# Kernel optimization log

Hardware: AMD Instinct MI355X
Metric: run time of the kernel (lower is better)

Reference implementation:

```python
import jax, jax.numpy as jnp
import numpy as np
import math

DIM = 1024
N_HEAD = 16
HEAD_DIM = DIM // N_HEAD  # 64
B, T = 4, 2048


def rotate_half(x):
    # lucidrains-style interleaved rotation: (x1, x2) pairs -> (-x2, x1)
    x = x.reshape(*x.shape[:-1], -1, 2)
    x1, x2 = x[..., 0], x[..., 1]
    return jnp.stack((-x2, x1), axis=-1).reshape(*x.shape[:-2], -1)


def apply_rope(x):
    # x: [b, h, t, d]
    d = x.shape[-1]
    t = x.shape[-2]
    inv_freq = 1.0 / (10000.0 ** (jnp.arange(0, d, 2, dtype=jnp.float32) / d))  # [d/2]
    angles = jnp.arange(t, dtype=jnp.float32)[:, None] * inv_freq[None, :]      # [t, d/2]
    angles = jnp.repeat(angles, 2, axis=-1)                                     # [t, d] interleaved
    cos, sin = jnp.cos(angles), jnp.sin(angles)
    return x * cos + rotate_half(x) * sin


def setup_inputs() -> dict:
    key = jax.random.key(0)
    kx, kw1, kb1, kw2, kb2 = jax.random.split(key, 5)
    x = jax.random.normal(kx, (B, T, DIM), dtype=jnp.float32)
    mask = jnp.tril(jnp.ones((T, T), dtype=jnp.int32))  # causal
    s = 0.02
    qkv_w = jax.random.normal(kw1, (DIM, 3 * DIM), dtype=jnp.float32) * s
    qkv_b = jax.random.normal(kb1, (3 * DIM,), dtype=jnp.float32) * s
    out_w = jax.random.normal(kw2, (DIM, DIM), dtype=jnp.float32) * s
    out_b = jax.random.normal(kb2, (DIM,), dtype=jnp.float32) * s
    return {"x": x, "mask": mask, "qkv_w": qkv_w, "qkv_b": qkv_b,
            "out_w": out_w, "out_b": out_b}


def reference(x, mask, qkv_w, qkv_b, out_w, out_b):
    b, t, _ = x.shape
    qkv = x @ qkv_w + qkv_b                       # [b, t, 3*dim]
    q, k, v = jnp.split(qkv, 3, axis=-1)
    def to_heads(z):
        return z.reshape(b, t, N_HEAD, HEAD_DIM).transpose(0, 2, 1, 3)  # [b,h,t,d]
    q, k, v = to_heads(q), to_heads(k), to_heads(v)
    q = apply_rope(q)
    k = apply_rope(k)
    scores = jnp.einsum('bhqd,bhkd->bhqk', q, k) / math.sqrt(HEAD_DIM)
    scores = jnp.where(mask[None, None, :, :] == 0, -jnp.inf, scores)
    attn = jax.nn.softmax(scores, axis=-1)        # dropout = identity (eval)
    out = jnp.einsum('bhqk,bhkd->bhqd', attn, v)  # [b,h,t,d]
    out = out.transpose(0, 2, 1, 3).reshape(b, t, DIM)
    return out @ out_w + out_b
```

## Files before the change

kernel.cpp:

```cpp
#include <hip/hip_runtime.h>

typedef __bf16 bf16_t;
typedef __bf16 bf16x8 __attribute__((ext_vector_type(8)));
typedef float  f32x4  __attribute__((ext_vector_type(4)));
typedef float  f32x16 __attribute__((ext_vector_type(16)));
typedef unsigned u32x4 __attribute__((ext_vector_type(4)));

#define DIMM  1024
#define NHEAD 16
#define HDIM  64
#define BATCH 4
#define SEQ   2048
#define MROWS (BATCH*SEQ)

#define AQB   128
#define AKV   64
#define NP    (SEQ/AQB)
#define SKS   72
#define LOG2E 1.44269504088896f

__device__ __forceinline__ void gload_lds16(const bf16_t* g, bf16_t* l) {
  __builtin_amdgcn_global_load_lds(
      (const __attribute__((address_space(1))) void*)g,
      (__attribute__((address_space(3))) void*)l, 16, 0, 0);
}

__device__ __forceinline__ unsigned short f2bu(float f) {
  bf16_t b = (bf16_t)f;
  return __builtin_bit_cast(unsigned short, b);
}
__device__ __forceinline__ float bu2f(unsigned short u) {
  return __uint_as_float(((unsigned)u) << 16);
}
__device__ __forceinline__ unsigned packbf(float a, float b) {
  return (unsigned)f2bu(a) | ((unsigned)f2bu(b) << 16);
}
__device__ __forceinline__ float fexp2(float x) {
  float r; asm("v_exp_f32 %0, %1" : "=v"(r) : "v"(x)); return r;
}

__global__ void k_convert(const float* __restrict__ in, bf16_t* __restrict__ out, int n4) {
  int i = blockIdx.x * blockDim.x + threadIdx.x;
  if (i >= n4) return;
  float4 v = reinterpret_cast<const float4*>(in)[i];
  ushort4 o;
  o.x = f2bu(v.x); o.y = f2bu(v.y); o.z = f2bu(v.z); o.w = f2bu(v.w);
  reinterpret_cast<ushort4*>(out)[i] = o;
}

__global__ void k_transpose_convert(const float* __restrict__ in, bf16_t* __restrict__ out,
                                    int R, int C) {
  __shared__ float tile[32][33];
  int cb = blockIdx.x * 32, rb = blockIdx.y * 32;
  int tx = threadIdx.x, ty = threadIdx.y;
  #pragma unroll
  for (int i = 0; i < 4; ++i)
    tile[ty + i*8][tx] = in[(size_t)(rb + ty + i*8) * C + cb + tx];
  __syncthreads();
  #pragma unroll
  for (int i = 0; i < 4; ++i)
    out[(size_t)(cb + ty + i*8) * R + rb + tx] = (bf16_t)tile[tx][ty + i*8];
}

__global__ void k_rope_table(float* __restrict__ cosT, float* __restrict__ sinT) {
  int id = blockIdx.x * blockDim.x + threadIdx.x;
  if (id >= SEQ * 32) return;
  int t = id >> 5, i = id & 31;
  double ang = (double)t * pow(10000.0, -(double)i / 32.0);
  cosT[id] = (float)cos(ang);
  sinT[id] = (float)sin(ang);
}

__global__ __launch_bounds__(512, 2) void k_gemm0(
    const bf16_t* __restrict__ A, const bf16_t* __restrict__ BT,
    const float* __restrict__ bias,
    bf16_t* __restrict__ q, bf16_t* __restrict__ k, bf16_t* __restrict__ vt,
    const float* __restrict__ cosT, const float* __restrict__ sinT)
{
  __shared__ bf16_t sA[2][2][128 * 64];
  __shared__ bf16_t sB[2][2][128 * 64];

  const int tid = threadIdx.x;
  const int w = tid >> 6;
  const int lane = tid & 63;
  const int wm = w >> 2, wn = w & 3;
  const int l15 = lane & 15, l4 = lane >> 4;

  int nwg = gridDim.x * gridDim.y;
  int id  = blockIdx.y * gridDim.x + blockIdx.x;
  int cpx = nwg >> 3;
  int sid = (id & 7) * cpx + (id >> 3);
  int bx = sid % gridDim.x, by = sid / gridDim.x;
  const int rowA0 = by * 256, colB0 = bx * 256;

  f32x4 acc[8][4] = {};
  bf16x8 bf_[4];

  auto stage = [&](int tile, int part) {
    if (tile >= 16) return;
    const int kh = part >> 1;
    const bool isB = part & 1;
    const bf16_t* src = isB ? BT : A;
    const int r0 = isB ? colB0 : rowA0;
    bf16_t* dst = (isB ? &sB[0][0][0] : &sA[0][0][0]) + ((tile & 1) * 2 + kh) * (128 * 64);
    #pragma unroll
    for (int call = 0; call < 2; ++call) {
      int n = call * 512 + tid;
      int R = n >> 3, slot = n & 7;
      int sp = slot ^ (R & 7);
      int row = R * 2 + (sp >> 2);
      gload_lds16(src + (size_t)(r0 + row) * 1024 + tile * 64 + kh * 32 + (sp & 3) * 8,
                  dst + n * 8);
    }
  };

  auto rdA = [&](int bc, int kh, int mfa) -> bf16x8 {
    int row = wm * 128 + mfa * 16 + l15;
    int R = row >> 1;
    int slot = (((row & 1) << 2) | l4) ^ (R & 7);
    return *reinterpret_cast<const bf16x8*>(&sA[bc][kh][R * 64 + slot * 8]);
  };
  auto rdB = [&](int bc, int kh, int nf) -> bf16x8 {
    int row = wn * 64 + nf * 16 + l15;
    int R = row >> 1;
    int slot = (((row & 1) << 2) | l4) ^ (R & 7);
    return *reinterpret_cast<const bf16x8*>(&sB[bc][kh][R * 64 + slot * 8]);
  };

  auto phase = [&](int bc, int kh, int mh, int stile, int spart, int wait_n) {
    bf16x8 af[4];
    if (mh == 0) {
      #pragma unroll
      for (int nf = 0; nf < 4; ++nf) bf_[nf] = rdB(bc, kh, nf);
    }
    #pragma unroll
    for (int mf = 0; mf < 4; ++mf) af[mf] = rdA(bc, kh, mh * 4 + mf);
    stage(stile, spart);
    if (wait_n == 4)      asm volatile("s_waitcnt vmcnt(4)" ::: "memory");
    else if (wait_n == 0) asm volatile("s_waitcnt vmcnt(0)" ::: "memory");
    __builtin_amdgcn_s_barrier();
    __builtin_amdgcn_s_setprio(1);
    #pragma unroll
    for (int mf = 0; mf < 4; ++mf)
      #pragma unroll
      for (int nf = 0; nf < 4; ++nf)
        acc[mh * 4 + mf][nf] = __builtin_amdgcn_mfma_f32_16x16x32_bf16(
            af[mf], bf_[nf], acc[mh * 4 + mf][nf], 0, 0, 0);
    __builtin_amdgcn_s_setprio(0);
    __builtin_amdgcn_s_barrier();
  };

  stage(0, 0); stage(0, 1); stage(0, 2); stage(0, 3);
  stage(1, 0); stage(1, 1);
  asm volatile("s_waitcnt vmcnt(4)" ::: "memory");
  __builtin_amdgcn_s_barrier();

  for (int i = 0; i < 8; ++i) {
    const int t0 = 2 * i, t1 = 2 * i + 1;
    phase(0, 0, 0, t1,     2, -1);
    phase(0, 0, 1, t1,     3, -1);
    phase(0, 1, 0, t0 + 2, 0, -1);
    phase(0, 1, 1, t0 + 2, 1, (t0 + 2 < 16) ? 4 : 0);
    phase(1, 0, 0, t0 + 2, 2, -1);
    phase(1, 0, 1, t0 + 2, 3, -1);
    phase(1, 1, 0, t0 + 3, 0, -1);
    phase(1, 1, 1, t0 + 3, 1, (t0 + 3 < 16) ? 4 : 0);
  }

  const bool isV = (bx >= 8);
  const bool isQ = (bx < 4);
  const float qs = 0.125f * LOG2E;
  if (isV) {
    #pragma unroll
    for (int mfa = 0; mfa < 8; ++mfa) {
      #pragma unroll
      for (int nf = 0; nf < 4; ++nf) {
        int n = colB0 + wn * 64 + nf * 16 + l15;
        int h = (n >> 6) & 15, d = n & 63;
        float bs = bias[n];
        int m0 = rowA0 + wm * 128 + mfa * 16 + l4 * 4;
        int b = m0 >> 11, t = m0 & 2047;
        ushort4 pk;
        pk.x = f2bu(acc[mfa][nf][0] + bs);
        pk.y = f2bu(acc[mfa][nf][1] + bs);
        pk.z = f2bu(acc[mfa][nf][2] + bs);
        pk.w = f2bu(acc[mfa][nf][3] + bs);
        *reinterpret_cast<ushort4*>(
            vt + ((size_t)((b * NHEAD + h) * HDIM + d)) * SEQ + t) = pk;
      }
    }
  } else {
    bf16_t* dst = isQ ? q : k;
    #pragma unroll
    for (int mfa = 0; mfa < 8; ++mfa) {
      #pragma unroll
      for (int nf = 0; nf < 4; ++nf) {
        int n = colB0 + wn * 64 + nf * 16 + l15;
        int h = (n >> 6) & 15, d = n & 63;
        int i2 = d >> 1;
        float bs = bias[n];
        #pragma unroll
        for (int r = 0; r < 4; ++r) {
          int m = rowA0 + wm * 128 + mfa * 16 + l4 * 4 + r;
          int b = m >> 11, t = m & 2047;
          float val = acc[mfa][nf][r] + bs;
          float prt = __shfl_xor(val, 1);
          float c = cosT[(t << 5) + i2], s = sinT[(t << 5) + i2];
          float y = (d & 1) ? (val * c + prt * s) : (val * c - prt * s);
          if (isQ) y *= qs;
          dst[((size_t)(b * NHEAD + h) * SEQ + t) * HDIM + d] = (bf16_t)y;
        }
      }
    }
  }
}

__global__ __launch_bounds__(256) void k_gemm1(
    const bf16_t* __restrict__ A, const bf16_t* __restrict__ BT,
    const float* __restrict__ bias, float* __restrict__ outf, int M, int N, int K)
{
  __shared__ bf16_t sA[128 * 32];
  __shared__ bf16_t sB[128 * 32];
  const int tid = threadIdx.x;
  const int w = tid >> 6, lane = tid & 63;
  const int wr = w >> 1, wc = w & 1;
  const int l15 = lane & 15, l4 = lane >> 4;

  int nwg = gridDim.x * gridDim.y;
  int id  = blockIdx.y * gridDim.x + blockIdx.x;
  int cpx = nwg >> 3;
  int sid = (id & 7) * cpx + (id >> 3);
  int bx = sid % gridDim.x, by = sid / gridDim.x;

  const int rowA0 = by * 128;
  const int colB0 = bx * 128;

  f32x4 acc[4][4] = {};

  const int nkt = K >> 5;
  for (int kt = 0; kt < nkt; ++kt) {
    __syncthreads();
    #pragma unroll
    for (int i = 0; i < 2; ++i) {
      int c = i * 256 + w * 64 + lane;
      int row = c >> 2, k8 = (c & 3) * 8;
      gload_lds16(A  + (size_t)(rowA0 + row) * K + kt * 32 + k8, sA + (i * 256 + w * 64) * 8);
      gload_lds16(BT + (size_t)(colB0 + row) * K + kt * 32 + k8, sB + (i * 256 + w * 64) * 8);
    }
    asm volatile("s_waitcnt vmcnt(0)" ::: "memory");
    __syncthreads();
    bf16x8 af[4], bfr[4];
    #pragma unroll
    for (int mi = 0; mi < 4; ++mi)
      af[mi] = *reinterpret_cast<const bf16x8*>(sA + (wr * 64 + mi * 16 + l15) * 32 + l4 * 8);
    #pragma unroll
    for (int ni = 0; ni < 4; ++ni)
      bfr[ni] = *reinterpret_cast<const bf16x8*>(sB + (wc * 64 + ni * 16 + l15) * 32 + l4 * 8);
    #pragma unroll
    for (int mi = 0; mi < 4; ++mi)
      #pragma unroll
      for (int ni = 0; ni < 4; ++ni)
        acc[mi][ni] = __builtin_amdgcn_mfma_f32_16x16x32_bf16(af[mi], bfr[ni], acc[mi][ni], 0, 0, 0);
  }

  #pragma unroll
  for (int mi = 0; mi < 4; ++mi) {
    #pragma unroll
    for (int ni = 0; ni < 4; ++ni) {
      int n = colB0 + wc * 64 + ni * 16 + l15;
      float bs = bias[n];
      #pragma unroll
      for (int r = 0; r < 4; ++r) {
        int m = rowA0 + wr * 64 + mi * 16 + l4 * 4 + r;
        outf[(size_t)m * N + n] = acc[mi][ni][r] + bs;
      }
    }
  }
}

__global__ __launch_bounds__(256, 2) void k_attn(
    const bf16_t* __restrict__ Q, const bf16_t* __restrict__ Kb,
    const bf16_t* __restrict__ Vt, bf16_t* __restrict__ O)
{
  __shared__ bf16_t sK[2][64 * SKS];
  __shared__ bf16_t sV[2][64 * SKS];

  const int tid = threadIdx.x;
  const int w = tid >> 6, lane = tid & 63;
  const int l31 = lane & 31, hi = lane >> 5;

  const int id = blockIdx.x;
  const int j4 = id >> 8;
  const int k4 = (id >> 6) & 3;
  const int bh = id & 63;
  const int qblk = (j4 == 0) ? 15 - 2 * k4
                 : (j4 == 1) ? 2 * k4
                 : (j4 == 2) ? 14 - 2 * k4
                 :             2 * k4 + 1;

  const size_t hbase = (size_t)bh * SEQ * HDIM;
  const int b = bh >> 4, h = bh & 15;
  const int srow = tid >> 3, sslot = tid & 7;

  const int qbase = qblk * AQB + 32 * w;
  const int nt = 2 * qblk + 2;

  bf16x8 qf[4];
  #pragma unroll
  for (int kt = 0; kt < 4; ++kt)
    qf[kt] = *reinterpret_cast<const bf16x8*>(
        Q + hbase + (size_t)(qbase + l31) * HDIM + kt * 16 + hi * 8);
  asm volatile("s_waitcnt vmcnt(0)" ::: "memory");
  asm volatile("" : "+v"(qf[0]), "+v"(qf[1]), "+v"(qf[2]), "+v"(qf[3]));

  u32x4 kr[2], vr[2];
  auto issue = [&](int t) {
    const bf16_t* kp = Kb + hbase + (size_t)(t * AKV + srow) * HDIM + sslot * 8;
    const bf16_t* vp = Vt + hbase + (size_t)srow * SEQ + t * AKV + sslot * 8;
    asm volatile("global_load_dwordx4 %0, %1, off" : "=v"(kr[0]) : "v"(kp));
    asm volatile("global_load_dwordx4 %0, %1, off" : "=v"(kr[1]) : "v"(kp + 32 * HDIM));
    asm volatile("global_load_dwordx4 %0, %1, off" : "=v"(vr[0]) : "v"(vp));
    asm volatile("global_load_dwordx4 %0, %1, off" : "=v"(vr[1]) : "v"(vp + 32 * SEQ));
  };
  auto stage = [&](int nb) {
    #pragma unroll
    for (int cc = 0; cc < 2; ++cc) {
      int row = srow + 32 * cc;
      *reinterpret_cast<u32x4*>(&sK[nb][row * SKS + ((sslot ^ (row >> 3)) << 3)]) = kr[cc];
      *reinterpret_cast<u32x4*>(&sV[nb][row * SKS + ((sslot ^ (row >> 3)) << 3)]) = vr[cc];
    }
  };

  float mrun = -1e30f, lrun = 0.f;
  f32x16 accO[2] = {};

  issue(0);
  asm volatile("s_waitcnt vmcnt(0)" ::: "memory");
  stage(0);
  issue(1);
  asm volatile("s_waitcnt lgkmcnt(0)" ::: "memory");
  __builtin_amdgcn_s_barrier();
  asm volatile("" ::: "memory");

  for (int t = 0; t < nt; ++t) {
    const int c = t & 1;
    if (t + 1 < nt) {
      asm volatile("s_waitcnt vmcnt(0)" ::: "memory");
      stage(c ^ 1);
      if (t + 2 < nt) issue(t + 2);
    }
    const bool masked = (t * AKV + AKV - 1 > qbase);
    #pragma unroll
    for (int sub = 0; sub < 2; ++sub) {
      f32x16 sc = {};
      __builtin_amdgcn_s_setprio(1);
      #pragma unroll
      for (int kt = 0; kt < 4; ++kt) {
        int krow = 32 * sub + l31;
        bf16x8 kf = *reinterpret_cast<const bf16x8*>(
            &sK[c][krow * SKS + (((2 * kt + hi) ^ (krow >> 3)) << 3)]);
        sc = __builtin_amdgcn_mfma_f32_32x32x16_bf16(kf, qf[kt], sc, 0, 0, 0);
      }
      __builtin_amdgcn_s_setprio(0);

      float p[16];
      const int qa = qbase + l31;
      const int kb0 = t * AKV + 32 * sub + 4 * hi;
      #pragma unroll
      for (int r = 0; r < 16; ++r) {
        float s = sc[r];
        if (masked) {
          int kvi = kb0 + (r & 3) + 8 * (r >> 2);
          if (kvi > qa) s = -1e30f;
        }
        p[r] = s;
      }
      float m0 = fmaxf(fmaxf(p[0],  p[1]),  p[2]);
      float m1 = fmaxf(fmaxf(p[3],  p[4]),  p[5]);
      float m2 = fmaxf(fmaxf(p[6],  p[7]),  p[8]);
      float m3 = fmaxf(fmaxf(p[9],  p[10]), p[11]);
      float m4 = fmaxf(fmaxf(p[12], p[13]), p[14]);
      float mt = fmaxf(fmaxf(fmaxf(m0, m1), fmaxf(m2, m3)), fmaxf(m4, p[15]));
      mt = fmaxf(mt, __shfl_xor(mt, 32));
      if (!__all(mt <= mrun + 11.54f)) {
        float mnew = fmaxf(mrun, mt);
        float scl = fexp2(mrun - mnew);
        mrun = mnew;
        lrun *= scl;
        #pragma unroll
        for (int i = 0; i < 16; ++i) { accO[0][i] *= scl; accO[1][i] *= scl; }
      }
      float rs = 0.f;
      #pragma unroll
      for (int r = 0; r < 16; ++r) { p[r] = fexp2(p[r] - mrun); rs += p[r]; }
      lrun += rs + __shfl_xor(rs, 32);

      bf16x8 pf[2];
      #pragma unroll
      for (int kt = 0; kt < 2; ++kt) {
        unsigned P01 = packbf(p[8*kt+0], p[8*kt+1]);
        unsigned P23 = packbf(p[8*kt+2], p[8*kt+3]);
        unsigned P45 = packbf(p[8*kt+4], p[8*kt+5]);
        unsigned P67 = packbf(p[8*kt+6], p[8*kt+7]);
        unsigned ra = __shfl_xor(hi == 0 ? P45 : P01, 32);
        unsigned rb = __shfl_xor(hi == 0 ? P67 : P23, 32);
        unsigned dw0 = hi == 0 ? P01 : ra;
        unsigned dw1 = hi == 0 ? P23 : rb;
        unsigned dw2 = hi == 0 ? ra : P45;
        unsigned dw3 = hi == 0 ? rb : P67;
        pf[kt] = __builtin_bit_cast(bf16x8, (u32x4){dw0, dw1, dw2, dw3});
      }

      __builtin_amdgcn_s_setprio(1);
      #pragma unroll
      for (int dt = 0; dt < 2; ++dt) {
        #pragma unroll
        for (int kt = 0; kt < 2; ++kt) {
          int vrow = 32 * dt + l31;
          bf16x8 vf = *reinterpret_cast<const bf16x8*>(
              &sV[c][vrow * SKS + (((4 * sub + 2 * kt + hi) ^ (vrow >> 3)) << 3)]);
          accO[dt] = __builtin_amdgcn_mfma_f32_32x32x16_bf16(vf, pf[kt], accO[dt], 0, 0, 0);
        }
      }
      __builtin_amdgcn_s_setprio(0);
    }
    asm volatile("s_waitcnt lgkmcnt(0)" ::: "memory");
    __builtin_amdgcn_s_barrier();
    asm volatile("" ::: "memory");
  }

  bf16_t* sOw = &sK[0][0] + w * (32 * SKS);
  float inv = 1.f / lrun;
  #pragma unroll
  for (int dt = 0; dt < 2; ++dt)
    #pragma unroll
    for (int r = 0; r < 16; ++r) {
      int d = 32 * dt + (r & 3) + 8 * (r >> 2) + 4 * hi;
      sOw[l31 * SKS + (d ^ ((l31 >> 3) << 3))] = (bf16_t)(accO[dt][r] * inv);
    }
  #pragma unroll
  for (int i = 0; i < 4; ++i) {
    int qr = 8 * i + (lane >> 3);
    int ch = lane & 7;
    bf16x8 vvv = *reinterpret_cast<const bf16x8*>(
        &sOw[qr * SKS + ((ch ^ (qr >> 3)) << 3)]);
    *reinterpret_cast<bf16x8*>(
        O + ((size_t)(b * SEQ + qbase + qr)) * DIMM + h * HDIM + ch * 8) = vvv;
  }
}

extern "C" void kernel_launch(void* const* d_in, const int* in_sizes, int n_in,
                              void* d_out, int out_size, void* d_ws, size_t ws_size,
                              hipStream_t stream) {
  const float* x     = (const float*)d_in[0];
  const float* qkv_w = (const float*)d_in[2];
  const float* qkv_b = (const float*)d_in[3];
  const float* out_w = (const float*)d_in[4];
  const float* out_b = (const float*)d_in[5];
  float* out = (float*)d_out;

  char* ws = (char*)d_ws;
  size_t off = 0;
  auto alloc = [&](size_t bytes) {
    char* p = ws + off;
    off += (bytes + 255) & ~(size_t)255;
    return (void*)p;
  };
  bf16_t* Xb    = (bf16_t*)alloc((size_t)MROWS * DIMM * 2);
  bf16_t* WqkvT = (bf16_t*)alloc((size_t)3 * DIMM * DIMM * 2);
  bf16_t* WoutT = (bf16_t*)alloc((size_t)DIMM * DIMM * 2);
  bf16_t* Qh    = (bf16_t*)alloc((size_t)64 * SEQ * HDIM * 2);
  bf16_t* Kh    = (bf16_t*)alloc((size_t)64 * SEQ * HDIM * 2);
  bf16_t* Vth   = (bf16_t*)alloc((size_t)64 * HDIM * SEQ * 2);
  bf16_t* AO    = (bf16_t*)alloc((size_t)MROWS * DIMM * 2);
  float*  cosT  = (float*)alloc((size_t)SEQ * 32 * 4);
  float*  sinT  = (float*)alloc((size_t)SEQ * 32 * 4);

  k_convert<<<(MROWS * DIMM / 4 + 255) / 256, 256, 0, stream>>>(x, Xb, MROWS * DIMM / 4);
  k_transpose_convert<<<dim3(3 * DIMM / 32, DIMM / 32), dim3(32, 8), 0, stream>>>(qkv_w, WqkvT, DIMM, 3 * DIMM);
  k_transpose_convert<<<dim3(DIMM / 32, DIMM / 32), dim3(32, 8), 0, stream>>>(out_w, WoutT, DIMM, DIMM);
  k_rope_table<<<(SEQ * 32 + 255) / 256, 256, 0, stream>>>(cosT, sinT);

  k_gemm0<<<dim3(3 * DIMM / 256, MROWS / 256), 512, 0, stream>>>(
      Xb, WqkvT, qkv_b, Qh, Kh, Vth, cosT, sinT);

  k_attn<<<dim3(NP * 64), 256, 0, stream>>>(Qh, Kh, Vth, AO);

  k_gemm1<<<dim3(DIMM / 128, MROWS / 128), 256, 0, stream>>>(
      AO, WoutT, out_b, out, MROWS, DIMM, DIMM);
}
```

Baseline: 195.6 us.

## Split long causal attention blocks across KV halves, drop LDS staging, add merge kernel

Query blocks 8-15 of the causal attention now have their KV range split into two halves, each run by a separate workgroup. The partial outputs and their running max and sum are written to scratch (reusing the bf16 X buffer), and a new merge kernel combines them. This balances work across 1536 workgroups. The attention kernel also reads K and V fragments straight from global memory into registers instead of double-buffering through LDS with barriers, and processes 64 keys per softmax step. The QKV GEMM pipeline waits are loosened to vmcnt(8), keeping more loads in flight. The costs are an extra launch, extra partial-result traffic, and uncached, possibly uncoalesced global fragment loads.

```diff
diff --git a/kernel.cpp b/kernel.cpp
--- a/kernel.cpp
+++ b/kernel.cpp
@@ -18,6 +18,9 @@
 #define NP    (SEQ/AQB)
 #define SKS   72
 #define LOG2E 1.44269504088896f
+
+__device__ const int d_qb[24] = {15,15,7,14,14,13,13,6,12,12,11,11,5,10,10,9,9,4,8,8,3,2,1,0};
+__device__ const int d_hh[24] = { 0, 1,2, 0, 1, 0, 1,2, 0, 1, 0, 1,2, 0, 1,0,1,2,0,1,2,2,2,2};
 
 __device__ __forceinline__ void gload_lds16(const bf16_t* g, bf16_t* l) {
   __builtin_amdgcn_global_load_lds(
@@ -136,7 +139,8 @@
     #pragma unroll
     for (int mf = 0; mf < 4; ++mf) af[mf] = rdA(bc, kh, mh * 4 + mf);
     stage(stile, spart);
-    if (wait_n == 4)      asm volatile("s_waitcnt vmcnt(4)" ::: "memory");
+    if (wait_n == 8)      asm volatile("s_waitcnt vmcnt(8)" ::: "memory");
+    else if (wait_n == 4) asm volatile("s_waitcnt vmcnt(4)" ::: "memory");
     else if (wait_n == 0) asm volatile("s_waitcnt vmcnt(0)" ::: "memory");
     __builtin_amdgcn_s_barrier();
     __builtin_amdgcn_s_setprio(1);
@@ -157,14 +161,15 @@
 
   for (int i = 0; i < 8; ++i) {
     const int t0 = 2 * i, t1 = 2 * i + 1;
+    const bool mid = (t0 + 2 < 16);
     phase(0, 0, 0, t1,     2, -1);
-    phase(0, 0, 1, t1,     3, -1);
+    phase(0, 0, 1, t1,     3, 8);
     phase(0, 1, 0, t0 + 2, 0, -1);
-    phase(0, 1, 1, t0 + 2, 1, (t0 + 2 < 16) ? 4 : 0);
+    phase(0, 1, 1, t0 + 2, 1, mid ? 8 : 4);
     phase(1, 0, 0, t0 + 2, 2, -1);
-    phase(1, 0, 1, t0 + 2, 3, -1);
+    phase(1, 0, 1, t0 + 2, 3, mid ? 8 : 0);
     phase(1, 1, 0, t0 + 3, 0, -1);
-    phase(1, 1, 1, t0 + 3, 1, (t0 + 3 < 16) ? 4 : 0);
+    phase(1, 1, 1, t0 + 3, 1, (t0 + 3 < 16) ? 8 : 0);
   }
 
   const bool isV = (bx >= 8);
@@ -280,156 +285,132 @@
 
 __global__ __launch_bounds__(256, 2) void k_attn(
     const bf16_t* __restrict__ Q, const bf16_t* __restrict__ Kb,
-    const bf16_t* __restrict__ Vt, bf16_t* __restrict__ O)
+    const bf16_t* __restrict__ Vt, bf16_t* __restrict__ O,
+    bf16_t* __restrict__ Opart, float* __restrict__ ml)
 {
-  __shared__ bf16_t sK[2][64 * SKS];
-  __shared__ bf16_t sV[2][64 * SKS];
+  __shared__ bf16_t sO[4][32 * SKS];
 
   const int tid = threadIdx.x;
   const int w = tid >> 6, lane = tid & 63;
   const int l31 = lane & 31, hi = lane >> 5;
 
   const int id = blockIdx.x;
-  const int j4 = id >> 8;
-  const int k4 = (id >> 6) & 3;
+  const int cls = id >> 6;
   const int bh = id & 63;
-  const int qblk = (j4 == 0) ? 15 - 2 * k4
-                 : (j4 == 1) ? 2 * k4
-                 : (j4 == 2) ? 14 - 2 * k4
-                 :             2 * k4 + 1;
+  const int qblk = d_qb[cls];
+  const int hh = d_hh[cls];
+  const int ntf = 2 * qblk + 2;
+  const int t0 = (hh == 1) ? (ntf >> 1) : 0;
+  const int t1 = (hh == 0) ? (ntf >> 1) : ntf;
 
   const size_t hbase = (size_t)bh * SEQ * HDIM;
   const int b = bh >> 4, h = bh & 15;
-  const int srow = tid >> 3, sslot = tid & 7;
-
   const int qbase = qblk * AQB + 32 * w;
-  const int nt = 2 * qblk + 2;
 
   bf16x8 qf[4];
   #pragma unroll
   for (int kt = 0; kt < 4; ++kt)
     qf[kt] = *reinterpret_cast<const bf16x8*>(
         Q + hbase + (size_t)(qbase + l31) * HDIM + kt * 16 + hi * 8);
-  asm volatile("s_waitcnt vmcnt(0)" ::: "memory");
-  asm volatile("" : "+v"(qf[0]), "+v"(qf[1]), "+v"(qf[2]), "+v"(qf[3]));
-
-  u32x4 kr[2], vr[2];
-  auto issue = [&](int t) {
-    const bf16_t* kp = Kb + hbase + (size_t)(t * AKV + srow) * HDIM + sslot * 8;
-    const bf16_t* vp = Vt + hbase + (size_t)srow * SEQ + t * AKV + sslot * 8;
-    asm volatile("global_load_dwordx4 %0, %1, off" : "=v"(kr[0]) : "v"(kp));
-    asm volatile("global_load_dwordx4 %0, %1, off" : "=v"(kr[1]) : "v"(kp + 32 * HDIM));
-    asm volatile("global_load_dwordx4 %0, %1, off" : "=v"(vr[0]) : "v"(vp));
-    asm volatile("global_load_dwordx4 %0, %1, off" : "=v"(vr[1]) : "v"(vp + 32 * SEQ));
-  };
-  auto stage = [&](int nb) {
-    #pragma unroll
-    for (int cc = 0; cc < 2; ++cc) {
-      int row = srow + 32 * cc;
-      *reinterpret_cast<u32x4*>(&sK[nb][row * SKS + ((sslot ^ (row >> 3)) << 3)]) = kr[cc];
-      *reinterpret_cast<u32x4*>(&sV[nb][row * SKS + ((sslot ^ (row >> 3)) << 3)]) = vr[cc];
-    }
-  };
 
   float mrun = -1e30f, lrun = 0.f;
   f32x16 accO[2] = {};
 
-  issue(0);
-  asm volatile("s_waitcnt vmcnt(0)" ::: "memory");
-  stage(0);
-  issue(1);
-  asm volatile("s_waitcnt lgkmcnt(0)" ::: "memory");
-  __builtin_amdgcn_s_barrier();
-  asm volatile("" ::: "memory");
-
-  for (int t = 0; t < nt; ++t) {
-    const int c = t & 1;
-    if (t + 1 < nt) {
-      asm volatile("s_waitcnt vmcnt(0)" ::: "memory");
-      stage(c ^ 1);
-      if (t + 2 < nt) issue(t + 2);
-    }
+  const bf16_t* Kl = Kb + hbase + (size_t)l31 * HDIM + hi * 8;
+  const bf16_t* Vl = Vt + hbase + (size_t)l31 * SEQ;
+
+  for (int t = t0; t < t1; ++t) {
     const bool masked = (t * AKV + AKV - 1 > qbase);
-    #pragma unroll
-    for (int sub = 0; sub < 2; ++sub) {
-      f32x16 sc = {};
-      __builtin_amdgcn_s_setprio(1);
-      #pragma unroll
-      for (int kt = 0; kt < 4; ++kt) {
-        int krow = 32 * sub + l31;
-        bf16x8 kf = *reinterpret_cast<const bf16x8*>(
-            &sK[c][krow * SKS + (((2 * kt + hi) ^ (krow >> 3)) << 3)]);
-        sc = __builtin_amdgcn_mfma_f32_32x32x16_bf16(kf, qf[kt], sc, 0, 0, 0);
+    const bf16_t* kp = Kl + (size_t)t * AKV * HDIM;
+
+    f32x16 s0 = {}, s1 = {};
+    __builtin_amdgcn_s_setprio(1);
+    #pragma unroll
+    for (int kt = 0; kt < 4; ++kt) {
+      bf16x8 kf0 = *reinterpret_cast<const bf16x8*>(kp + kt * 16);
+      s0 = __builtin_amdgcn_mfma_f32_32x32x16_bf16(kf0, qf[kt], s0, 0, 0, 0);
+    }
+    #pragma unroll
+    for (int kt = 0; kt < 4; ++kt) {
+      bf16x8 kf1 = *reinterpret_cast<const bf16x8*>(kp + 32 * HDIM + kt * 16);
+      s1 = __builtin_amdgcn_mfma_f32_32x32x16_bf16(kf1, qf[kt], s1, 0, 0, 0);
+    }
+    __builtin_amdgcn_s_setprio(0);
+
+    const int qa = qbase + l31;
+    const int kb0 = t * AKV + 4 * hi;
+    if (masked) {
+      #pragma unroll
+      for (int r = 0; r < 16; ++r) {
+        int kvi = kb0 + (r & 3) + 8 * (r >> 2);
+        if (kvi > qa) s0[r] = -1e30f;
+        if (kvi + 32 > qa) s1[r] = -1e30f;
       }
-      __builtin_amdgcn_s_setprio(0);
-
-      float p[16];
-      const int qa = qbase + l31;
-      const int kb0 = t * AKV + 32 * sub + 4 * hi;
-      #pragma unroll
-      for (int r = 0; r < 16; ++r) {
-        float s = sc[r];
-        if (masked) {
-          int kvi = kb0 + (r & 3) + 8 * (r >> 2);
-          if (kvi > qa) s = -1e30f;
-        }
-        p[r] = s;
+    }
+    float mm[16];
+    #pragma unroll
+    for (int r = 0; r < 16; ++r) mm[r] = fmaxf(s0[r], s1[r]);
+    float m0_ = fmaxf(fmaxf(mm[0],  mm[1]),  mm[2]);
+    float m1_ = fmaxf(fmaxf(mm[3],  mm[4]),  mm[5]);
+    float m2_ = fmaxf(fmaxf(mm[6],  mm[7]),  mm[8]);
+    float m3_ = fmaxf(fmaxf(mm[9],  mm[10]), mm[11]);
+    float m4_ = fmaxf(fmaxf(mm[12], mm[13]), mm[14]);
+    float mt = fmaxf(fmaxf(fmaxf(m0_, m1_), fmaxf(m2_, m3_)), fmaxf(m4_, mm[15]));
+    mt = fmaxf(mt, __shfl_xor(mt, 32));
+    if (!__all(mt <= mrun + 11.54f)) {
+      float mnew = fmaxf(mrun, mt);
+      float scl = fexp2(mrun - mnew);
+      mrun = mnew;
+      lrun *= scl;
+      #pragma unroll
+      for (int i = 0; i < 16; ++i) { accO[0][i] *= scl; accO[1][i] *= scl; }
+    }
+    float rs = 0.f;
+    #pragma unroll
+    for (int r = 0; r < 16; ++r) { s0[r] = fexp2(s0[r] - mrun); rs += s0[r]; }
+    #pragma unroll
+    for (int r = 0; r < 16; ++r) { s1[r] = fexp2(s1[r] - mrun); rs += s1[r]; }
+    lrun += rs;
+
+    bf16x8 pf[4];
+    #pragma unroll
+    for (int ktt = 0; ktt < 4; ++ktt) {
+      const int bb = 8 * (ktt & 1);
+      unsigned P01, P23, P45, P67;
+      if (ktt < 2) {
+        P01 = packbf(s0[bb+0], s0[bb+1]); P23 = packbf(s0[bb+2], s0[bb+3]);
+        P45 = packbf(s0[bb+4], s0[bb+5]); P67 = packbf(s0[bb+6], s0[bb+7]);
+      } else {
+        P01 = packbf(s1[bb+0], s1[bb+1]); P23 = packbf(s1[bb+2], s1[bb+3]);
+        P45 = packbf(s1[bb+4], s1[bb+5]); P67 = packbf(s1[bb+6], s1[bb+7]);
       }
-      float m0 = fmaxf(fmaxf(p[0],  p[1]),  p[2]);
-      float m1 = fmaxf(fmaxf(p[3],  p[4]),  p[5]);
-      float m2 = fmaxf(fmaxf(p[6],  p[7]),  p[8]);
-      float m3 = fmaxf(fmaxf(p[9],  p[10]), p[11]);
-      float m4 = fmaxf(fmaxf(p[12], p[13]), p[14]);
-      float mt = fmaxf(fmaxf(fmaxf(m0, m1), fmaxf(m2, m3)), fmaxf(m4, p[15]));
-      mt = fmaxf(mt, __shfl_xor(mt, 32));
-      if (!__all(mt <= mrun + 11.54f)) {
-        float mnew = fmaxf(mrun, mt);
-        float scl = fexp2(mrun - mnew);
-        mrun = mnew;
-        lrun *= scl;
-        #pragma unroll
-        for (int i = 0; i < 16; ++i) { accO[0][i] *= scl; accO[1][i] *= scl; }
+      unsigned ra = __shfl_xor(hi == 0 ? P45 : P01, 32);
+      unsigned rb = __shfl_xor(hi == 0 ? P67 : P23, 32);
+      unsigned dw0 = hi == 0 ? P01 : ra;
+      unsigned dw1 = hi == 0 ? P23 : rb;
+      unsigned dw2 = hi == 0 ? ra : P45;
+      unsigned dw3 = hi == 0 ? rb : P67;
+      pf[ktt] = __builtin_bit_cast(bf16x8, (u32x4){dw0, dw1, dw2, dw3});
+    }
+
+    const bf16_t* vp = Vl + (size_t)t * AKV;
+    __builtin_amdgcn_s_setprio(1);
+    #pragma unroll
+    for (int dt = 0; dt < 2; ++dt) {
+      #pragma unroll
+      for (int ktt = 0; ktt < 4; ++ktt) {
+        int s = 4 * (ktt >> 1) + 2 * (ktt & 1) + hi;
+        bf16x8 vf = *reinterpret_cast<const bf16x8*>(
+            vp + (size_t)dt * 32 * SEQ + s * 8);
+        accO[dt] = __builtin_amdgcn_mfma_f32_32x32x16_bf16(vf, pf[ktt], accO[dt], 0, 0, 0);
       }
-      float rs = 0.f;
-      #pragma unroll
-      for (int r = 0; r < 16; ++r) { p[r] = fexp2(p[r] - mrun); rs += p[r]; }
-      lrun += rs + __shfl_xor(rs, 32);
-
-      bf16x8 pf[2];
-      #pragma unroll
-      for (int kt = 0; kt < 2; ++kt) {
-        unsigned P01 = packbf(p[8*kt+0], p[8*kt+1]);
-        unsigned P23 = packbf(p[8*kt+2], p[8*kt+3]);
-        unsigned P45 = packbf(p[8*kt+4], p[8*kt+5]);
-        unsigned P67 = packbf(p[8*kt+6], p[8*kt+7]);
-        unsigned ra = __shfl_xor(hi == 0 ? P45 : P01, 32);
-        unsigned rb = __shfl_xor(hi == 0 ? P67 : P23, 32);
-        unsigned dw0 = hi == 0 ? P01 : ra;
-        unsigned dw1 = hi == 0 ? P23 : rb;
-        unsigned dw2 = hi == 0 ? ra : P45;
-        unsigned dw3 = hi == 0 ? rb : P67;
-        pf[kt] = __builtin_bit_cast(bf16x8, (u32x4){dw0, dw1, dw2, dw3});
-      }
-
-      __builtin_amdgcn_s_setprio(1);
-      #pragma unroll
-      for (int dt = 0; dt < 2; ++dt) {
-        #pragma unroll
-        for (int kt = 0; kt < 2; ++kt) {
-          int vrow = 32 * dt + l31;
-          bf16x8 vf = *reinterpret_cast<const bf16x8*>(
-              &sV[c][vrow * SKS + (((4 * sub + 2 * kt + hi) ^ (vrow >> 3)) << 3)]);
-          accO[dt] = __builtin_amdgcn_mfma_f32_32x32x16_bf16(vf, pf[kt], accO[dt], 0, 0, 0);
-        }
-      }
-      __builtin_amdgcn_s_setprio(0);
-    }
-    asm volatile("s_waitcnt lgkmcnt(0)" ::: "memory");
-    __builtin_amdgcn_s_barrier();
-    asm volatile("" ::: "memory");
-  }
-
-  bf16_t* sOw = &sK[0][0] + w * (32 * SKS);
+    }
+    __builtin_amdgcn_s_setprio(0);
+  }
+
+  lrun += __shfl_xor(lrun, 32);
+
+  bf16_t* sOw = &sO[w][0];
   float inv = 1.f / lrun;
   #pragma unroll
   for (int dt = 0; dt < 2; ++dt)
@@ -438,14 +419,68 @@
       int d = 32 * dt + (r & 3) + 8 * (r >> 2) + 4 * hi;
       sOw[l31 * SKS + (d ^ ((l31 >> 3) << 3))] = (bf16_t)(accO[dt][r] * inv);
     }
+  if (hh == 2) {
+    #pragma unroll
+    for (int i = 0; i < 4; ++i) {
+      int qr = 8 * i + (lane >> 3);
+      int ch = lane & 7;
+      bf16x8 vvv = *reinterpret_cast<const bf16x8*>(
+          &sOw[qr * SKS + ((ch ^ (qr >> 3)) << 3)]);
+      *reinterpret_cast<bf16x8*>(
+          O + ((size_t)(b * SEQ + qbase + qr)) * DIMM + h * HDIM + ch * 8) = vvv;
+    }
+  } else {
+    const int pb = ((qblk - 8) * 2 + hh) * 64 + bh;
+    #pragma unroll
+    for (int i = 0; i < 4; ++i) {
+      int qr = 8 * i + (lane >> 3);
+      int ch = lane & 7;
+      bf16x8 vvv = *reinterpret_cast<const bf16x8*>(
+          &sOw[qr * SKS + ((ch ^ (qr >> 3)) << 3)]);
+      *reinterpret_cast<bf16x8*>(
+          Opart + ((size_t)pb * 128 + 32 * w + qr) * 64 + ch * 8) = vvv;
+    }
+    if (hi == 0) {
+      size_t mi = ((size_t)pb * 128 + 32 * w + l31) * 2;
+      ml[mi] = mrun; ml[mi + 1] = lrun;
+    }
+  }
+}
+
+__global__ __launch_bounds__(256) void k_merge(
+    const bf16_t* __restrict__ Opart, const float* __restrict__ ml,
+    bf16_t* __restrict__ O)
+{
+  int blk = blockIdx.x;
+  int qi = blk >> 6;
+  int bh = blk & 63;
+  int b = bh >> 4, h = bh & 15;
+  int qblk = qi + 8;
+  int base0 = (qi * 2 + 0) * 64 + bh;
+  int base1 = (qi * 2 + 1) * 64 + bh;
+  int q = threadIdx.x >> 1;
+  int d0 = (threadIdx.x & 1) * 32;
+
+  float m0 = ml[((size_t)base0 * 128 + q) * 2], l0 = ml[((size_t)base0 * 128 + q) * 2 + 1];
+  float m1 = ml[((size_t)base1 * 128 + q) * 2], l1 = ml[((size_t)base1 * 128 + q) * 2 + 1];
+  float m = fmaxf(m0, m1);
+  float w0 = fexp2(m0 - m) * l0;
+  float w1 = fexp2(m1 - m) * l1;
+  float inv = 1.f / (w0 + w1);
+  w0 *= inv; w1 *= inv;
+
+  const bf16_t* p0 = Opart + ((size_t)base0 * 128 + q) * 64 + d0;
+  const bf16_t* p1 = Opart + ((size_t)base1 * 128 + q) * 64 + d0;
+  bf16_t* po = O + ((size_t)(b * SEQ + qblk * 128 + q)) * DIMM + h * HDIM + d0;
   #pragma unroll
   for (int i = 0; i < 4; ++i) {
-    int qr = 8 * i + (lane >> 3);
-    int ch = lane & 7;
-    bf16x8 vvv = *reinterpret_cast<const bf16x8*>(
-        &sOw[qr * SKS + ((ch ^ (qr >> 3)) << 3)]);
-    *reinterpret_cast<bf16x8*>(
-        O + ((size_t)(b * SEQ + qbase + qr)) * DIMM + h * HDIM + ch * 8) = vvv;
+    bf16x8 a = *reinterpret_cast<const bf16x8*>(p0 + i * 8);
+    bf16x8 c = *reinterpret_cast<const bf16x8*>(p1 + i * 8);
+    bf16x8 o;
+    #pragma unroll
+    for (int j = 0; j < 8; ++j)
+      o[j] = (bf16_t)(w0 * (float)a[j] + w1 * (float)c[j]);
+    *reinterpret_cast<bf16x8*>(po + i * 8) = o;
   }
 }
 
@@ -475,6 +510,8 @@
   bf16_t* AO    = (bf16_t*)alloc((size_t)MROWS * DIMM * 2);
   float*  cosT  = (float*)alloc((size_t)SEQ * 32 * 4);
   float*  sinT  = (float*)alloc((size_t)SEQ * 32 * 4);
+  float*  mlbuf = (float*)alloc((size_t)16 * 64 * 128 * 2 * 4);
+  bf16_t* Opart = Xb;
 
   k_convert<<<(MROWS * DIMM / 4 + 255) / 256, 256, 0, stream>>>(x, Xb, MROWS * DIMM / 4);
   k_transpose_convert<<<dim3(3 * DIMM / 32, DIMM / 32), dim3(32, 8), 0, stream>>>(qkv_w, WqkvT, DIMM, 3 * DIMM);
@@ -484,7 +521,9 @@
   k_gemm0<<<dim3(3 * DIMM / 256, MROWS / 256), 512, 0, stream>>>(
       Xb, WqkvT, qkv_b, Qh, Kh, Vth, cosT, sinT);
 
-  k_attn<<<dim3(NP * 64), 256, 0, stream>>>(Qh, Kh, Vth, AO);
+  k_attn<<<dim3(24 * 64), 256, 0, stream>>>(Qh, Kh, Vth, AO, Opart, mlbuf);
+
+  k_merge<<<dim3(512), 256, 0, stream>>>(Opart, mlbuf, AO);
 
   k_gemm1<<<dim3(DIMM / 128, MROWS / 128), 256, 0, stream>>>(
       AO, WoutT, out_b, out, MROWS, DIMM, DIMM);
```

Measured after the change: 267.7 us. 36.9% more time.
